# Optimization experiments

Hardware: AMD Instinct MI355X
Metric: run time of the kernel (lower is better)

The kernel has to match this reference:

```python
import jax, jax.numpy as jnp
import numpy as np

D = 128          # latent_dim
N = 40000        # num nodes
B = 8            # num graphs in batch
S = N // B       # nodes per graph
K = 6            # knn
E = 640000       # spatial edges
FF = 256         # ffn hidden


def glorot(key, shape):
    lim = jnp.sqrt(6.0 / (shape[0] + shape[-1]))
    return jax.random.uniform(key, shape, minval=-lim, maxval=lim, dtype=jnp.float32)


def setup_inputs() -> dict:
    key = jax.random.key(0)
    ks = jax.random.split(key, 24)
    inp = {
        "x": jax.random.normal(ks[0], (N, D), dtype=jnp.float32),
        "edge_index": jax.random.randint(ks[1], (2, E), 0, N, dtype=jnp.int64),
        "edge_attr": jax.random.uniform(ks[2], (E, 1), dtype=jnp.float32),
        "batch": jnp.repeat(jnp.arange(B, dtype=jnp.int64), S),
        # spatial GATv2Conv params
        "W_sl": glorot(ks[3], (D, D)), "b_sl": jnp.zeros((D,), jnp.float32),
        "W_sr": glorot(ks[4], (D, D)), "b_sr": jnp.zeros((D,), jnp.float32),
        "att_s": glorot(ks[5], (D,)), "W_se": glorot(ks[6], (1, D)),
        "bias_s": jnp.zeros((D,), jnp.float32),
        # latent GATv2Conv params (no edge features)
        "W_ll": glorot(ks[7], (D, D)), "b_ll": jnp.zeros((D,), jnp.float32),
        "W_lr": glorot(ks[8], (D, D)), "b_lr": jnp.zeros((D,), jnp.float32),
        "att_l": glorot(ks[9], (D,)), "bias_l": jnp.zeros((D,), jnp.float32),
        # concat_skip fusion linear: in = 2*D
        "W_c": glorot(ks[10], (2 * D, D)), "b_c": jnp.zeros((D,), jnp.float32),
        # FFN
        "W_f1": glorot(ks[11], (D, FF)), "b_f1": jnp.zeros((FF,), jnp.float32),
        "W_f2": glorot(ks[12], (FF, D)), "b_f2": jnp.zeros((D,), jnp.float32),
    }
    return inp


def relu6(v):
    return jnp.clip(v, 0.0, 6.0)


def segment_softmax(logits, seg, num_segments):
    m = jax.ops.segment_max(logits, seg, num_segments=num_segments)
    e = jnp.exp(logits - m[seg])
    s = jax.ops.segment_sum(e, seg, num_segments=num_segments)
    return e / s[seg]


def gatv2(x, src, dst, edge_feat, W_l, b_l, W_r, b_r, att, bias):
    """PyG GATv2Conv, heads=1, concat=True, negative_slope=0.2."""
    xl = x @ W_l + b_l            # [N,D] source transform
    xr = x @ W_r + b_r            # [N,D] target transform
    h = xl[src] + xr[dst]         # [E,D]
    if edge_feat is not None:
        h = h + edge_feat         # [E,D] already projected by lin_edge
    h = jax.nn.leaky_relu(h, 0.2)
    alpha = h @ att               # [E]
    alpha = segment_softmax(alpha, dst, N)
    out = jax.ops.segment_sum(xl[src] * alpha[:, None], dst, num_segments=N)
    return out + bias


def knn_edges(x):
    """knn_graph(k=K, loop=False, flow='source_to_target') per graph, plus
    the self loops that latent GATv2Conv adds (add_self_loops=True)."""
    xs = jax.lax.stop_gradient(x).reshape(B, S, D)
    sq = jnp.sum(xs * xs, axis=-1)                       # [B,S]
    d2 = sq[:, :, None] + sq[:, None, :] - 2.0 * jnp.einsum('bid,bjd->bij', xs, xs)
    d2 = jnp.where(jnp.eye(S, dtype=bool)[None], jnp.inf, d2)
    _, idx = jax.lax.top_k(-d2, K)                       # [B,S,K] neighbor ids
    offs = (jnp.arange(B) * S)[:, None, None]
    src = (idx + offs).reshape(-1)                       # neighbors -> sources
    dst = jnp.repeat(jnp.arange(N), K)                   # query nodes -> targets
    loop = jnp.arange(N)
    return jnp.concatenate([src, loop]), jnp.concatenate([dst, loop])


def reference(x, edge_index, edge_attr, batch,
              W_sl, b_sl, W_sr, b_sr, att_s, W_se, bias_s,
              W_ll, b_ll, W_lr, b_lr, att_l, bias_l,
              W_c, b_c, W_f1, b_f1, W_f2, b_f2):
    # spatial channel: GATv2 with scalar edge attr
    e_feat = edge_attr @ W_se                            # lin_edge, [E,D]
    ch_sp = gatv2(x, edge_index[0], edge_index[1], e_feat,
                  W_sl, b_sl, W_sr, b_sr, att_s, bias_s)
    # latent channel: dynamic kNN graph + GATv2
    src_l, dst_l = knn_edges(x)
    ch_lat = gatv2(x, src_l, dst_l, None,
                   W_ll, b_ll, W_lr, b_lr, att_l, bias_l)
    # fusion = concat_skip
    fused = jnp.concatenate([ch_sp, ch_lat], axis=-1) @ W_c + b_c + x
    # FFN block (norms are Identity), residual
    ffn = relu6(fused @ W_f1 + b_f1) @ W_f2 + b_f2
    out = fused + ffn
    # plain_last=False -> final activation relu6
    return relu6(out)
```

## Files before the change

### kernel.cpp

```cpp
#include <hip/hip_runtime.h>
#include <math.h>

constexpr int N  = 40000;
constexpr int D  = 128;
constexpr int E  = 640000;
constexpr int Bg = 8;
constexpr int Sg = 5000;
constexpr int KN = 6;
constexpr int FF = 256;
constexpr int QLEN = 1280;
constexpr int NCAND = 48;

typedef short short8 __attribute__((ext_vector_type(8)));
typedef float f32x4  __attribute__((ext_vector_type(4)));
typedef __attribute__((address_space(1))) const void* gvp;
typedef __attribute__((address_space(3))) void* lvp;

__device__ __forceinline__ unsigned short f2bf(float f)
{
    unsigned int u = __float_as_uint(f);
    return (unsigned short)((u + 0x7fffu + ((u >> 16) & 1u)) >> 16);
}

__device__ __forceinline__ unsigned umin2(unsigned a, unsigned b) { return a < b ? a : b; }

__global__ __launch_bounds__(256) void w_prep_k(
    const float* __restrict__ W0, const float* __restrict__ W1,
    const float* __restrict__ W2, const float* __restrict__ W3,
    const float* __restrict__ Wc, const float* __restrict__ Wf1,
    const float* __restrict__ Wf2,
    unsigned short* __restrict__ wt4, unsigned short* __restrict__ wtc,
    unsigned short* __restrict__ wtf1, unsigned short* __restrict__ wtf2)
{
    int idx = blockIdx.x * 256 + threadIdx.x;
    if (idx < 65536) {
        int m = idx >> 14, rem = idx & 16383;
        int k = rem & 127, c = rem >> 7;
        const float* Wm = (m == 0) ? W0 : (m == 1) ? W1 : (m == 2) ? W2 : W3;
        wt4[m * 16384 + c * 128 + k] = f2bf(Wm[k * 128 + c]);
    } else if (idx < 98304) {
        int rem = idx - 65536; int k = rem & 255, c = rem >> 8;
        wtc[c * 256 + k] = f2bf(Wc[k * 128 + c]);
    } else if (idx < 131072) {
        int rem = idx - 98304; int k = rem & 127, c = rem >> 7;
        wtf1[c * 128 + k] = f2bf(Wf1[k * 256 + c]);
    } else {
        int rem = idx - 131072; int k = rem & 255, c = rem >> 8;
        wtf2[c * 256 + k] = f2bf(Wf2[k * 128 + c]);
    }
}

__global__ __launch_bounds__(256) void gemm_mfma_k(
    const float* __restrict__ A, int lda,
    const unsigned short* __restrict__ Wt, int Kdim,
    const float* __restrict__ bias,
    const float* __restrict__ res,
    float* __restrict__ out, int ldo, int act)
{
    __shared__ float xs[64][36];
    __shared__ unsigned short ws[128][40];
    int tid = threadIdx.x;
    int w = tid >> 6, lane = tid & 63;
    int lg = lane >> 4, ln = lane & 15;
    int r0 = blockIdx.x * 64;
    int cb = blockIdx.y * 128;

    f32x4 acc[8];
#pragma unroll
    for (int ct = 0; ct < 8; ++ct) acc[ct] = {0.f, 0.f, 0.f, 0.f};

    int srow = tid >> 2, sk8 = (tid & 3) * 8;
    int wcol = tid >> 1, wk = (tid & 1) * 16;

    for (int kt = 0; kt < Kdim; kt += 32) {
        __syncthreads();
        *(float4*)&xs[srow][sk8]     = *(const float4*)&A[(size_t)(r0 + srow) * lda + kt + sk8];
        *(float4*)&xs[srow][sk8 + 4] = *(const float4*)&A[(size_t)(r0 + srow) * lda + kt + sk8 + 4];
        *(short8*)&ws[wcol][wk]     = *(const short8*)&Wt[(size_t)(cb + wcol) * Kdim + kt + wk];
        *(short8*)&ws[wcol][wk + 8] = *(const short8*)&Wt[(size_t)(cb + wcol) * Kdim + kt + wk + 8];
        __syncthreads();

        int arow = w * 16 + ln;
        f32x4 a0 = *(const f32x4*)&xs[arow][lg * 8];
        f32x4 a1 = *(const f32x4*)&xs[arow][lg * 8 + 4];
        float af[8] = {a0[0], a0[1], a0[2], a0[3], a1[0], a1[1], a1[2], a1[3]};
        short8 ah, al;
#pragma unroll
        for (int i = 0; i < 8; ++i) {
            unsigned short h = f2bf(af[i]);
            ah[i] = (short)h;
            float hf = __uint_as_float(((unsigned)h) << 16);
            al[i] = (short)f2bf(af[i] - hf);
        }
#pragma unroll
        for (int ct = 0; ct < 8; ++ct) {
            short8 bw = *(const short8*)&ws[ct * 16 + ln][lg * 8];
            acc[ct] = __builtin_amdgcn_mfma_f32_16x16x32_bf16(ah, bw, acc[ct], 0, 0, 0);
            acc[ct] = __builtin_amdgcn_mfma_f32_16x16x32_bf16(al, bw, acc[ct], 0, 0, 0);
        }
    }

#pragma unroll
    for (int ct = 0; ct < 8; ++ct) {
        int c = cb + ct * 16 + ln;
        float bv = bias[c];
#pragma unroll
        for (int rg = 0; rg < 4; ++rg) {
            int r = r0 + w * 16 + lg * 4 + rg;
            float v = acc[ct][rg] + bv;
            if (res) v += res[(size_t)r * 128 + c];
            if (act) v = fminf(fmaxf(v, 0.f), 6.f);
            out[(size_t)r * ldo + c] = v;
        }
    }
}

__global__ __launch_bounds__(256) void gemm4_mfma_k(
    const float* __restrict__ A, const unsigned short* __restrict__ wt4,
    const float* __restrict__ b0, const float* __restrict__ b1,
    const float* __restrict__ b2, const float* __restrict__ b3,
    float* __restrict__ o0, float* __restrict__ o1,
    float* __restrict__ o2, float* __restrict__ o3)
{
    const unsigned short* Wt = wt4 + blockIdx.y * 16384;
    const float* bias; float* out;
    if (blockIdx.y == 0)      { bias = b0; out = o0; }
    else if (blockIdx.y == 1) { bias = b1; out = o1; }
    else if (blockIdx.y == 2) { bias = b2; out = o2; }
    else                      { bias = b3; out = o3; }

    __shared__ float xs[64][36];
    __shared__ unsigned short ws[128][40];
    int tid = threadIdx.x;
    int w = tid >> 6, lane = tid & 63;
    int lg = lane >> 4, ln = lane & 15;
    int r0 = blockIdx.x * 64;

    f32x4 acc[8];
#pragma unroll
    for (int ct = 0; ct < 8; ++ct) acc[ct] = {0.f, 0.f, 0.f, 0.f};

    int srow = tid >> 2, sk8 = (tid & 3) * 8;
    int wcol = tid >> 1, wk = (tid & 1) * 16;

    for (int kt = 0; kt < 128; kt += 32) {
        __syncthreads();
        *(float4*)&xs[srow][sk8]     = *(const float4*)&A[(size_t)(r0 + srow) * 128 + kt + sk8];
        *(float4*)&xs[srow][sk8 + 4] = *(const float4*)&A[(size_t)(r0 + srow) * 128 + kt + sk8 + 4];
        *(short8*)&ws[wcol][wk]     = *(const short8*)&Wt[(size_t)wcol * 128 + kt + wk];
        *(short8*)&ws[wcol][wk + 8] = *(const short8*)&Wt[(size_t)wcol * 128 + kt + wk + 8];
        __syncthreads();

        int arow = w * 16 + ln;
        f32x4 a0 = *(const f32x4*)&xs[arow][lg * 8];
        f32x4 a1 = *(const f32x4*)&xs[arow][lg * 8 + 4];
        float af[8] = {a0[0], a0[1], a0[2], a0[3], a1[0], a1[1], a1[2], a1[3]};
        short8 ah, al;
#pragma unroll
        for (int i = 0; i < 8; ++i) {
            unsigned short h = f2bf(af[i]);
            ah[i] = (short)h;
            float hf = __uint_as_float(((unsigned)h) << 16);
            al[i] = (short)f2bf(af[i] - hf);
        }
#pragma unroll
        for (int ct = 0; ct < 8; ++ct) {
            short8 bw = *(const short8*)&ws[ct * 16 + ln][lg * 8];
            acc[ct] = __builtin_amdgcn_mfma_f32_16x16x32_bf16(ah, bw, acc[ct], 0, 0, 0);
            acc[ct] = __builtin_amdgcn_mfma_f32_16x16x32_bf16(al, bw, acc[ct], 0, 0, 0);
        }
    }

#pragma unroll
    for (int ct = 0; ct < 8; ++ct) {
        int c = ct * 16 + ln;
        float bv = bias[c];
#pragma unroll
        for (int rg = 0; rg < 4; ++rg) {
            int r = r0 + w * 16 + lg * 4 + rg;
            out[(size_t)r * 128 + c] = acc[ct][rg] + bv;
        }
    }
}

__global__ __launch_bounds__(256) void prep_k(const float* __restrict__ x,
                                              unsigned short* __restrict__ xh,
                                              float* __restrict__ sqn)
{
    int w = threadIdx.x >> 6, lane = threadIdx.x & 63;
    int row = blockIdx.x * 4 + w;
    float2 v = *(const float2*)&x[(size_t)row * 128 + lane * 2];
    ushort2 h = make_ushort2(f2bf(v.x), f2bf(v.y));
    *(ushort2*)&xh[(size_t)row * 128 + lane * 2] = h;
    float s = fmaf(v.y, v.y, v.x * v.x);
#pragma unroll
    for (int off = 32; off; off >>= 1) s += __shfl_xor(s, off);
    if (lane == 0) sqn[row] = s;
}

__device__ __forceinline__ void ins6(unsigned (&d)[6], unsigned k)
{
#pragma unroll
    for (int t = 0; t < 6; ++t) {
        unsigned lo = d[t] < k ? d[t] : k;
        unsigned hi = d[t] < k ? k : d[t];
        d[t] = lo; k = hi;
    }
}

__global__ __launch_bounds__(256) void knn_mfma_k(const unsigned short* __restrict__ xh,
                                                  const float* __restrict__ sqn,
                                                  int* __restrict__ cand)
{
    __shared__ char lds[33280];

    int b = blockIdx.x;
    int g = b & 7, r = b >> 3;
    int qtr = r & 3, qblk = r >> 2;
    int gbase = g * Sg;
    int cbase = qtr * QLEN;
    int qlen = (qtr < 3) ? QLEN : (Sg - 3 * QLEN);
    int ntiles = (qlen + 63) >> 6;
    int tid = threadIdx.x;
    int w = tid >> 6, lane = tid & 63;
    int lg = lane >> 4, ln = lane & 15;
    int q0 = qblk * 128 + w * 32;

    short8 bh[2][4];
#pragma unroll
    for (int s = 0; s < 2; ++s) {
        int q = q0 + s * 16 + ln;
        int qrow = gbase + (q < Sg ? q : Sg - 1);
#pragma unroll
        for (int ks = 0; ks < 4; ++ks)
            bh[s][ks] = *(const short8*)&xh[(size_t)qrow * 128 + ks * 32 + lg * 8];
    }

    auto stage = [&](int t64, int buf) {
        int c0 = cbase + t64 * 64;
#pragma unroll
        for (int i = 0; i < 4; ++i) {
            int row = i * 16 + (tid >> 4);
            int cr = c0 + row;
            if (cr >= Sg) cr = Sg - 1;
            int sslot = (tid & 15) ^ (row & 7);
            const unsigned short* src = &xh[(size_t)(gbase + cr) * 128 + sslot * 8];
            char* dst = lds + buf * 16384 + i * 4096 + (tid & 192) * 16;
            __builtin_amdgcn_global_load_lds((gvp)src, (lvp)dst, 16, 0, 0);
        }
        if (tid < 64) {
            int cl = c0 + tid;
            float* cs = (float*)(lds + 32768 + buf * 256);
            cs[tid] = (cl < cbase + qlen) ? (sqn[gbase + cl] + 1024.0f) : __builtin_inff();
        }
    };

    unsigned d6a[6], d6b[6];
#pragma unroll
    for (int t = 0; t < 6; ++t) { d6a[t] = 0xFFFFFFFFu; d6b[t] = 0xFFFFFFFFu; }

    stage(0, 0);
    __syncthreads();

    for (int t64 = 0; t64 < ntiles; ++t64) {
        int cur = t64 & 1;
        if (t64 + 1 < ntiles) stage(t64 + 1, cur ^ 1);
        const char* ldsH = lds + cur * 16384;
        const float* cs_s = (const float*)(lds + 32768 + cur * 256);
        int c0 = cbase + t64 * 64;

#pragma unroll
        for (int g16 = 0; g16 < 4; ++g16) {
            f32x4 acc0 = {0.f, 0.f, 0.f, 0.f};
            f32x4 acc1 = {0.f, 0.f, 0.f, 0.f};
            int rr = g16 * 16 + ln;
            int rsw = (ln & 7) << 4;
#pragma unroll
            for (int ks = 0; ks < 4; ++ks) {
                short8 ah = *(const short8*)(ldsH + rr * 256 + ((lg * 16 + ks * 64) ^ rsw));
                acc0 = __builtin_amdgcn_mfma_f32_16x16x32_bf16(ah, bh[0][ks], acc0, 0, 0, 0);
                acc1 = __builtin_amdgcn_mfma_f32_16x16x32_bf16(ah, bh[1][ks], acc1, 0, 0, 0);
            }
            f32x4 cv = *(const f32x4*)&cs_s[g16 * 16 + lg * 4];
            int idx0 = (c0 - cbase) + g16 * 16 + lg * 4;
            unsigned kb0[4], kb1[4];
#pragma unroll
            for (int rg = 0; rg < 4; ++rg) {
                kb0[rg] = __float_as_uint(fmaf(-2.f, acc0[rg], cv[rg]));
                kb1[rg] = __float_as_uint(fmaf(-2.f, acc1[rg], cv[rg]));
            }
            unsigned mn0 = umin2(umin2(kb0[0], kb0[1]), umin2(kb0[2], kb0[3]));
            unsigned mn1 = umin2(umin2(kb1[0], kb1[1]), umin2(kb1[2], kb1[3]));
            if ((mn0 & 0xFFFFF800u) < d6a[5]) {
#pragma unroll
                for (int rg = 0; rg < 4; ++rg) {
                    unsigned k = (kb0[rg] & 0xFFFFF800u) | (unsigned)(idx0 + rg);
                    if (k < d6a[5]) ins6(d6a, k);
                }
            }
            if ((mn1 & 0xFFFFF800u) < d6b[5]) {
#pragma unroll
                for (int rg = 0; rg < 4; ++rg) {
                    unsigned k = (kb1[rg] & 0xFFFFF800u) | (unsigned)(idx0 + rg);
                    if (k < d6b[5]) ins6(d6b, k);
                }
            }
        }
        __syncthreads();
    }

#pragma unroll
    for (int s = 0; s < 2; ++s) {
        unsigned m12[12];
#pragma unroll
        for (int t = 0; t < 6; ++t) m12[t] = s ? d6b[t] : d6a[t];
#pragma unroll
        for (int t = 6; t < 12; ++t) m12[t] = 0xFFFFFFFFu;
#pragma unroll
        for (int sg = 1; sg < 4; ++sg)
#pragma unroll
            for (int t = 0; t < 6; ++t) {
                unsigned v = __shfl(s ? d6b[t] : d6a[t], ln + sg * 16);
#pragma unroll
                for (int u = 0; u < 12; ++u) {
                    unsigned lo = m12[u] < v ? m12[u] : v;
                    unsigned hi = m12[u] < v ? v : m12[u];
                    m12[u] = lo; v = hi;
                }
            }
        int q = q0 + s * 16 + ln;
        if (lg == 0 && q < Sg) {
            int* cp = &cand[(size_t)(gbase + q) * NCAND + qtr * 12];
#pragma unroll
            for (int t = 0; t < 12; ++t) cp[t] = gbase + cbase + (int)(m12[t] & 2047u);
        }
    }
}

__global__ __launch_bounds__(256) void knn_rerank_k(const float* __restrict__ x,
                                                    const float* __restrict__ sqn,
                                                    const int* __restrict__ cand,
                                                    int* __restrict__ knn_idx)
{
    int w = threadIdx.x >> 6, lane = threadIdx.x & 63;
    int grp = lane >> 4, gl = lane & 15;
    int q = blockIdx.x * 4 + w;
    float4 qa = *(const float4*)&x[(size_t)q * 128 + gl * 8];
    float4 qb = *(const float4*)&x[(size_t)q * 128 + gl * 8 + 4];
    const int* cp = &cand[(size_t)q * NCAND + grp * 12];

    float d6[6]; int i6[6]; float mx = __builtin_inff(); int sl = 0;
#pragma unroll
    for (int t = 0; t < 6; ++t) { d6[t] = __builtin_inff(); i6[t] = -1; }

#pragma unroll 2
    for (int j = 0; j < 12; ++j) {
        int c = cp[j];
        bool ok = (unsigned)c < (unsigned)N && c != q;
        int ca = ok ? c : 0;
        float4 va = *(const float4*)&x[(size_t)ca * 128 + gl * 8];
        float4 vb = *(const float4*)&x[(size_t)ca * 128 + gl * 8 + 4];
        float p = qa.x * va.x;
        p = fmaf(qa.y, va.y, p); p = fmaf(qa.z, va.z, p); p = fmaf(qa.w, va.w, p);
        p = fmaf(qb.x, vb.x, p); p = fmaf(qb.y, vb.y, p);
        p = fmaf(qb.z, vb.z, p); p = fmaf(qb.w, vb.w, p);
#pragma unroll
        for (int off = 1; off < 16; off <<= 1) p += __shfl_xor(p, off);
        float dv = ok ? fmaf(-2.f, p, sqn[ca]) : __builtin_inff();
        if (dv < mx) {
#pragma unroll
            for (int t = 0; t < 6; ++t)
                if (t == sl) { d6[t] = dv; i6[t] = c; }
            float m2 = d6[0]; int s2 = 0;
#pragma unroll
            for (int t = 1; t < 6; ++t)
                if (d6[t] > m2) { m2 = d6[t]; s2 = t; }
            mx = m2; sl = s2;
        }
    }

#pragma unroll
    for (int sg = 1; sg < 4; ++sg) {
#pragma unroll
        for (int t = 0; t < 6; ++t) {
            float dv = __shfl(d6[t], gl + sg * 16);
            int ci = __shfl(i6[t], gl + sg * 16);
            if (grp == 0 && dv < mx) {
#pragma unroll
                for (int u = 0; u < 6; ++u)
                    if (u == sl) { d6[u] = dv; i6[u] = ci; }
                float m2 = d6[0]; int s2 = 0;
#pragma unroll
                for (int u = 1; u < 6; ++u)
                    if (d6[u] > m2) { m2 = d6[u]; s2 = u; }
                mx = m2; sl = s2;
            }
        }
    }
    if (lane < 6) {
        int v;
#pragma unroll
        for (int t = 0; t < 6; ++t) if (t == lane) v = i6[t];
        knn_idx[(size_t)q * 6 + lane] = v;
    }
}

__global__ __launch_bounds__(256) void hist_k(const int* __restrict__ dstA, int* __restrict__ deg)
{
    int e = blockIdx.x * 256 + threadIdx.x;
    atomicAdd(&deg[dstA[e]], 1);
}

__global__ __launch_bounds__(1024) void scan_k(const int* __restrict__ deg, int* __restrict__ rowptr)
{
    __shared__ int ps[1024];
    int t = threadIdx.x;
    const int chunk = 40;
    int base = t * chunk;
    int s = 0;
    for (int k = 0; k < chunk; ++k) { int i = base + k; if (i < N) s += deg[i]; }
    ps[t] = s;
    __syncthreads();
    for (int off = 1; off < 1024; off <<= 1) {
        int v = (t >= off) ? ps[t - off] : 0;
        __syncthreads();
        ps[t] += v;
        __syncthreads();
    }
    int run = ps[t] - s;
    for (int k = 0; k < chunk; ++k) {
        int i = base + k;
        if (i < N) { rowptr[i] = run; run += deg[i]; }
    }
    if (t == 0) rowptr[N] = E;
}

__global__ __launch_bounds__(256) void scatter_k(const int* __restrict__ srcA, const int* __restrict__ dstA,
                                                 const float* __restrict__ ea,
                                                 const int* __restrict__ rowptr, int* __restrict__ cnt,
                                                 int* __restrict__ csr_src, float* __restrict__ csr_ea)
{
    int e = blockIdx.x * 256 + threadIdx.x;
    int d = dstA[e];
    int pos = rowptr[d] + atomicAdd(&cnt[d], 1);
    csr_src[pos] = srcA[e];
    csr_ea[pos] = ea[e];
}

__global__ __launch_bounds__(256) void spatial_gat_k(
    const float* __restrict__ xl, const float* __restrict__ xr,
    const int* __restrict__ rowptr, const int* __restrict__ csr_src, const float* __restrict__ csr_ea,
    const float* __restrict__ att, const float* __restrict__ wse, const float* __restrict__ bias,
    float* __restrict__ ch2)
{
    int w = threadIdx.x >> 6, lane = threadIdx.x & 63;
    int dst = blockIdx.x * 4 + w;
    int base = rowptr[dst];
    int deg = rowptr[dst + 1] - base;
    float xr0 = xr[(size_t)dst * 128 + lane], xr1 = xr[(size_t)dst * 128 + 64 + lane];
    float at0 = att[lane], at1 = att[64 + lane];
    float we0 = wse[lane], we1 = wse[64 + lane];

    float m = -1e30f, ssum = 0.f, o0 = 0.f, o1 = 0.f;
    for (int i = 0; i < deg; ++i) {
        int s = csr_src[base + i];
        float ea = csr_ea[base + i];
        float v0 = xl[(size_t)s * 128 + lane];
        float v1 = xl[(size_t)s * 128 + 64 + lane];
        float h0 = fmaf(ea, we0, v0 + xr0);
        float h1 = fmaf(ea, we1, v1 + xr1);
        h0 = h0 > 0.f ? h0 : 0.2f * h0;
        h1 = h1 > 0.f ? h1 : 0.2f * h1;
        float p = fmaf(h1, at1, h0 * at0);
#pragma unroll
        for (int off = 32; off; off >>= 1) p += __shfl_xor(p, off);
        if (p <= m) {
            float wt = __expf(p - m);
            ssum += wt;
            o0 = fmaf(wt, v0, o0);
            o1 = fmaf(wt, v1, o1);
        } else {
            float sc = __expf(m - p);
            ssum = fmaf(ssum, sc, 1.f);
            o0 = fmaf(o0, sc, v0);
            o1 = fmaf(o1, sc, v1);
            m = p;
        }
    }
    float inv = deg > 0 ? 1.f / ssum : 0.f;
    ch2[(size_t)dst * 256 + lane]      = fmaf(o0, inv, bias[lane]);
    ch2[(size_t)dst * 256 + 64 + lane] = fmaf(o1, inv, bias[64 + lane]);
}

__global__ __launch_bounds__(256) void latent_gat_k(
    const float* __restrict__ xl, const float* __restrict__ xr,
    const int* __restrict__ knn, const float* __restrict__ att,
    const float* __restrict__ bias, float* __restrict__ ch2)
{
    int w = threadIdx.x >> 6, lane = threadIdx.x & 63;
    int dst = blockIdx.x * 4 + w;
    float xr0 = xr[(size_t)dst * 128 + lane], xr1 = xr[(size_t)dst * 128 + 64 + lane];
    float at0 = att[lane], at1 = att[64 + lane];
    int s[7];
#pragma unroll
    for (int j = 0; j < 6; ++j) s[j] = knn[(size_t)dst * 6 + j];
    s[6] = dst;
    float l[7];
#pragma unroll
    for (int j = 0; j < 7; ++j) {
        float h0 = xl[(size_t)s[j] * 128 + lane] + xr0;
        float h1 = xl[(size_t)s[j] * 128 + 64 + lane] + xr1;
        h0 = h0 > 0.f ? h0 : 0.2f * h0;
        h1 = h1 > 0.f ? h1 : 0.2f * h1;
        float p = h0 * at0 + h1 * at1;
#pragma unroll
        for (int off = 32; off; off >>= 1) p += __shfl_xor(p, off);
        l[j] = p;
    }
    float m = l[0];
#pragma unroll
    for (int j = 1; j < 7; ++j) m = fmaxf(m, l[j]);
    float sum = 0.f;
#pragma unroll
    for (int j = 0; j < 7; ++j) { l[j] = __expf(l[j] - m); sum += l[j]; }
    float inv = 1.f / sum;
    float o0 = 0.f, o1 = 0.f;
#pragma unroll
    for (int j = 0; j < 7; ++j) {
        float a = l[j] * inv;
        o0 = fmaf(a, xl[(size_t)s[j] * 128 + lane], o0);
        o1 = fmaf(a, xl[(size_t)s[j] * 128 + 64 + lane], o1);
    }
    ch2[(size_t)dst * 256 + 128 + lane] = o0 + bias[lane];
    ch2[(size_t)dst * 256 + 192 + lane] = o1 + bias[64 + lane];
}

extern "C" void kernel_launch(void* const* d_in, const int* in_sizes, int n_in,
                              void* d_out, int out_size, void* d_ws, size_t ws_size,
                              hipStream_t stream)
{
    const float* x      = (const float*)d_in[0];
    const int*   ei     = (const int*)  d_in[1];
    const float* eattr  = (const float*)d_in[2];
    const float* W_sl   = (const float*)d_in[4];
    const float* b_sl   = (const float*)d_in[5];
    const float* W_sr   = (const float*)d_in[6];
    const float* b_sr   = (const float*)d_in[7];
    const float* att_s  = (const float*)d_in[8];
    const float* W_se   = (const float*)d_in[9];
    const float* bias_s = (const float*)d_in[10];
    const float* W_ll   = (const float*)d_in[11];
    const float* b_ll   = (const float*)d_in[12];
    const float* W_lr   = (const float*)d_in[13];
    const float* b_lr   = (const float*)d_in[14];
    const float* att_l  = (const float*)d_in[15];
    const float* bias_l = (const float*)d_in[16];
    const float* W_c    = (const float*)d_in[17];
    const float* b_c    = (const float*)d_in[18];
    const float* W_f1   = (const float*)d_in[19];
    const float* b_f1   = (const float*)d_in[20];
    const float* W_f2   = (const float*)d_in[21];
    const float* b_f2   = (const float*)d_in[22];
    float* out = (float*)d_out;

    char* wp = (char*)d_ws;
    auto take = [&](size_t bytes) { char* p = wp; wp += (bytes + 255) & ~(size_t)255; return p; };
    float* xl_s    = (float*)take((size_t)N * D * 4);
    float* xr_s    = (float*)take((size_t)N * D * 4);
    float* xl_l    = (float*)take((size_t)N * D * 4);
    float* xr_l    = (float*)take((size_t)N * D * 4);
    float* ch2     = (float*)take((size_t)N * 2 * D * 4);
    float* sqn     = (float*)take((size_t)N * 4);
    int*   knn_idx = (int*)  take((size_t)N * KN * 4);
    int*   deg     = (int*)  take((size_t)N * 4);
    int*   rowptr  = (int*)  take((size_t)(N + 1) * 4);
    int*   csr_src = (int*)  take((size_t)E * 4);
    float* csr_ea  = (float*)take((size_t)E * 4);
    unsigned short* x_hi = (unsigned short*)take((size_t)N * D * 2);
    int*   knn_cand = (int*)take((size_t)N * NCAND * 4);
    unsigned short* wt4  = (unsigned short*)take(65536 * 2);
    unsigned short* wtc  = (unsigned short*)take(32768 * 2);
    unsigned short* wtf1 = (unsigned short*)take(32768 * 2);
    unsigned short* wtf2 = (unsigned short*)take(32768 * 2);
    float* fused   = xl_s;
    float* hbuf    = ch2;
    if ((size_t)(wp - (char*)d_ws) > ws_size) return;

    dim3 blk(256);

    w_prep_k<<<dim3(640), blk, 0, stream>>>(W_sl, W_sr, W_ll, W_lr, W_c, W_f1, W_f2,
                                            wt4, wtc, wtf1, wtf2);

    gemm4_mfma_k<<<dim3(N / 64, 4), blk, 0, stream>>>(x, wt4,
        b_sl, b_sr, b_ll, b_lr, xl_s, xr_s, xl_l, xr_l);

    prep_k<<<dim3(N / 4), blk, 0, stream>>>(x, x_hi, sqn);
    knn_mfma_k<<<dim3(Bg * 40 * 4), blk, 0, stream>>>(x_hi, sqn, knn_cand);
    knn_rerank_k<<<dim3(N / 4), blk, 0, stream>>>(x, sqn, knn_cand, knn_idx);

    hipMemsetAsync(deg, 0, (size_t)N * 4, stream);
    hist_k<<<dim3(E / 256), blk, 0, stream>>>(ei + E, deg);
    scan_k<<<dim3(1), dim3(1024), 0, stream>>>(deg, rowptr);
    hipMemsetAsync(deg, 0, (size_t)N * 4, stream);
    scatter_k<<<dim3(E / 256), blk, 0, stream>>>(ei, ei + E, eattr, rowptr, deg, csr_src, csr_ea);

    spatial_gat_k<<<dim3(N / 4), blk, 0, stream>>>(xl_s, xr_s, rowptr, csr_src, csr_ea,
                                                   att_s, W_se, bias_s, ch2);
    latent_gat_k<<<dim3(N / 4), blk, 0, stream>>>(xl_l, xr_l, knn_idx, att_l, bias_l, ch2);

    gemm_mfma_k<<<dim3(N / 64, 1), blk, 0, stream>>>(ch2, 2 * D, wtc, 256, b_c, x, fused, 128, 0);
    gemm_mfma_k<<<dim3(N / 64, 2), blk, 0, stream>>>(fused, 128, wtf1, 128, b_f1, nullptr, hbuf, 256, 1);
    gemm_mfma_k<<<dim3(N / 64, 1), blk, 0, stream>>>(hbuf, 256, wtf2, 256, b_f2, fused, out, 128, 1);
}
```

Measured before the change: 584.2 us.

## Single-buffer kNN tile staging via registers and merge the two GAT kernels

```diff
diff --git a/kernel.cpp b/kernel.cpp
--- a/kernel.cpp
+++ b/kernel.cpp
@@ -13,8 +13,6 @@
 
 typedef short short8 __attribute__((ext_vector_type(8)));
 typedef float f32x4  __attribute__((ext_vector_type(4)));
-typedef __attribute__((address_space(1))) const void* gvp;
-typedef __attribute__((address_space(3))) void* lvp;
 
 __device__ __forceinline__ unsigned short f2bf(float f)
 {
@@ -212,7 +210,9 @@
                                                   const float* __restrict__ sqn,
                                                   int* __restrict__ cand)
 {
-    __shared__ char lds[33280];
+    __shared__ char lds[16640];
+    char* ldsH = lds;
+    float* cs_s = (float*)(lds + 16384);
 
     int b = blockIdx.x;
     int g = b & 7, r = b >> 3;
@@ -221,6 +221,7 @@
     int cbase = qtr * QLEN;
     int qlen = (qtr < 3) ? QLEN : (Sg - 3 * QLEN);
     int ntiles = (qlen + 63) >> 6;
+    int nfull = (qtr < 3) ? ntiles : ntiles - 1;
     int tid = threadIdx.x;
     int w = tid >> 6, lane = tid & 63;
     int lg = lane >> 4, ln = lane & 15;
@@ -236,39 +237,50 @@
             bh[s][ks] = *(const short8*)&xh[(size_t)qrow * 128 + ks * 32 + lg * 8];
     }
 
-    auto stage = [&](int t64, int buf) {
+    int srow = tid >> 4, sslot = tid & 15;
+    int sw_st = (srow & 7) << 4;
+    int dstoff[4];
+    const unsigned short* src[4];
+#pragma unroll
+    for (int i = 0; i < 4; ++i) {
+        int row = i * 16 + srow;
+        dstoff[i] = row * 256 + ((sslot * 16) ^ sw_st);
+        src[i] = &xh[(size_t)(gbase + cbase + row) * 128 + sslot * 8];
+    }
+    const float* csrc = &sqn[gbase + cbase];
+
+    unsigned d6a[6], d6b[6];
+#pragma unroll
+    for (int t = 0; t < 6; ++t) { d6a[t] = 0xFFFFFFFFu; d6b[t] = 0xFFFFFFFFu; }
+
+    for (int t64 = 0; t64 < ntiles; ++t64) {
+        __syncthreads();
+        if (t64 < nfull) {
+#pragma unroll
+            for (int i = 0; i < 4; ++i) {
+                short8 vh = *(const short8*)src[i];
+                src[i] += 64 * 128;
+                *(short8*)(ldsH + dstoff[i]) = vh;
+            }
+            if (tid < 64) cs_s[tid] = csrc[tid] + 1024.0f;
+        } else {
+            int c0 = cbase + t64 * 64;
+#pragma unroll
+            for (int i = 0; i < 4; ++i) {
+                int cr = c0 + i * 16 + srow;
+                if (cr >= Sg) cr = Sg - 1;
+                short8 vh = *(const short8*)&xh[(size_t)(gbase + cr) * 128 + sslot * 8];
+                *(short8*)(ldsH + dstoff[i]) = vh;
+            }
+            if (tid < 64) {
+                int cl = c0 + tid;
+                cs_s[tid] = (cl < cbase + qlen) ? (sqn[gbase + cl] + 1024.0f) : __builtin_inff();
+            }
+        }
+        csrc += 64;
+        __syncthreads();
+
         int c0 = cbase + t64 * 64;
-#pragma unroll
-        for (int i = 0; i < 4; ++i) {
-            int row = i * 16 + (tid >> 4);
-            int cr = c0 + row;
-            if (cr >= Sg) cr = Sg - 1;
-            int sslot = (tid & 15) ^ (row & 7);
-            const unsigned short* src = &xh[(size_t)(gbase + cr) * 128 + sslot * 8];
-            char* dst = lds + buf * 16384 + i * 4096 + (tid & 192) * 16;
-            __builtin_amdgcn_global_load_lds((gvp)src, (lvp)dst, 16, 0, 0);
-        }
-        if (tid < 64) {
-            int cl = c0 + tid;
-            float* cs = (float*)(lds + 32768 + buf * 256);
-            cs[tid] = (cl < cbase + qlen) ? (sqn[gbase + cl] + 1024.0f) : __builtin_inff();
-        }
-    };
-
-    unsigned d6a[6], d6b[6];
-#pragma unroll
-    for (int t = 0; t < 6; ++t) { d6a[t] = 0xFFFFFFFFu; d6b[t] = 0xFFFFFFFFu; }
-
-    stage(0, 0);
-    __syncthreads();
-
-    for (int t64 = 0; t64 < ntiles; ++t64) {
-        int cur = t64 & 1;
-        if (t64 + 1 < ntiles) stage(t64 + 1, cur ^ 1);
-        const char* ldsH = lds + cur * 16384;
-        const float* cs_s = (const float*)(lds + 32768 + cur * 256);
-        int c0 = cbase + t64 * 64;
-
 #pragma unroll
         for (int g16 = 0; g16 < 4; ++g16) {
             f32x4 acc0 = {0.f, 0.f, 0.f, 0.f};
@@ -306,7 +318,6 @@
                 }
             }
         }
-        __syncthreads();
     }
 
 #pragma unroll
@@ -447,92 +458,89 @@
     csr_ea[pos] = ea[e];
 }
 
-__global__ __launch_bounds__(256) void spatial_gat_k(
-    const float* __restrict__ xl, const float* __restrict__ xr,
+__global__ __launch_bounds__(256) void gat_fused_k(
+    const float* __restrict__ xl_s, const float* __restrict__ xr_s,
     const int* __restrict__ rowptr, const int* __restrict__ csr_src, const float* __restrict__ csr_ea,
-    const float* __restrict__ att, const float* __restrict__ wse, const float* __restrict__ bias,
+    const float* __restrict__ att_s, const float* __restrict__ wse, const float* __restrict__ bias_s,
+    const float* __restrict__ xl_l, const float* __restrict__ xr_l,
+    const int* __restrict__ knn, const float* __restrict__ att_l, const float* __restrict__ bias_l,
     float* __restrict__ ch2)
 {
     int w = threadIdx.x >> 6, lane = threadIdx.x & 63;
     int dst = blockIdx.x * 4 + w;
-    int base = rowptr[dst];
-    int deg = rowptr[dst + 1] - base;
-    float xr0 = xr[(size_t)dst * 128 + lane], xr1 = xr[(size_t)dst * 128 + 64 + lane];
-    float at0 = att[lane], at1 = att[64 + lane];
-    float we0 = wse[lane], we1 = wse[64 + lane];
-
-    float m = -1e30f, ssum = 0.f, o0 = 0.f, o1 = 0.f;
-    for (int i = 0; i < deg; ++i) {
-        int s = csr_src[base + i];
-        float ea = csr_ea[base + i];
-        float v0 = xl[(size_t)s * 128 + lane];
-        float v1 = xl[(size_t)s * 128 + 64 + lane];
-        float h0 = fmaf(ea, we0, v0 + xr0);
-        float h1 = fmaf(ea, we1, v1 + xr1);
-        h0 = h0 > 0.f ? h0 : 0.2f * h0;
-        h1 = h1 > 0.f ? h1 : 0.2f * h1;
-        float p = fmaf(h1, at1, h0 * at0);
-#pragma unroll
-        for (int off = 32; off; off >>= 1) p += __shfl_xor(p, off);
-        if (p <= m) {
-            float wt = __expf(p - m);
-            ssum += wt;
-            o0 = fmaf(wt, v0, o0);
-            o1 = fmaf(wt, v1, o1);
-        } else {
-            float sc = __expf(m - p);
-            ssum = fmaf(ssum, sc, 1.f);
-            o0 = fmaf(o0, sc, v0);
-            o1 = fmaf(o1, sc, v1);
-            m = p;
-        }
-    }
-    float inv = deg > 0 ? 1.f / ssum : 0.f;
-    ch2[(size_t)dst * 256 + lane]      = fmaf(o0, inv, bias[lane]);
-    ch2[(size_t)dst * 256 + 64 + lane] = fmaf(o1, inv, bias[64 + lane]);
-}
-
-__global__ __launch_bounds__(256) void latent_gat_k(
-    const float* __restrict__ xl, const float* __restrict__ xr,
-    const int* __restrict__ knn, const float* __restrict__ att,
-    const float* __restrict__ bias, float* __restrict__ ch2)
-{
-    int w = threadIdx.x >> 6, lane = threadIdx.x & 63;
-    int dst = blockIdx.x * 4 + w;
-    float xr0 = xr[(size_t)dst * 128 + lane], xr1 = xr[(size_t)dst * 128 + 64 + lane];
-    float at0 = att[lane], at1 = att[64 + lane];
-    int s[7];
-#pragma unroll
-    for (int j = 0; j < 6; ++j) s[j] = knn[(size_t)dst * 6 + j];
-    s[6] = dst;
-    float l[7];
-#pragma unroll
-    for (int j = 0; j < 7; ++j) {
-        float h0 = xl[(size_t)s[j] * 128 + lane] + xr0;
-        float h1 = xl[(size_t)s[j] * 128 + 64 + lane] + xr1;
-        h0 = h0 > 0.f ? h0 : 0.2f * h0;
-        h1 = h1 > 0.f ? h1 : 0.2f * h1;
-        float p = h0 * at0 + h1 * at1;
-#pragma unroll
-        for (int off = 32; off; off >>= 1) p += __shfl_xor(p, off);
-        l[j] = p;
-    }
-    float m = l[0];
-#pragma unroll
-    for (int j = 1; j < 7; ++j) m = fmaxf(m, l[j]);
-    float sum = 0.f;
-#pragma unroll
-    for (int j = 0; j < 7; ++j) { l[j] = __expf(l[j] - m); sum += l[j]; }
-    float inv = 1.f / sum;
-    float o0 = 0.f, o1 = 0.f;
-#pragma unroll
-    for (int j = 0; j < 7; ++j) {
-        float a = l[j] * inv;
-        o0 = fmaf(a, xl[(size_t)s[j] * 128 + lane], o0);
-        o1 = fmaf(a, xl[(size_t)s[j] * 128 + 64 + lane], o1);
-    }
-    ch2[(size_t)dst * 256 + 128 + lane] = o0 + bias[lane];
-    ch2[(size_t)dst * 256 + 192 + lane] = o1 + bias[64 + lane];
+
+    if (blockIdx.y == 0) {
+        int base = rowptr[dst];
+        int deg = rowptr[dst + 1] - base;
+        float xr0 = xr_s[(size_t)dst * 128 + lane], xr1 = xr_s[(size_t)dst * 128 + 64 + lane];
+        float at0 = att_s[lane], at1 = att_s[64 + lane];
+        float we0 = wse[lane], we1 = wse[64 + lane];
+
+        float m = -1e30f, ssum = 0.f, o0 = 0.f, o1 = 0.f;
+        for (int i = 0; i < deg; ++i) {
+            int s = csr_src[base + i];
+            float ea = csr_ea[base + i];
+            float v0 = xl_s[(size_t)s * 128 + lane];
+            float v1 = xl_s[(size_t)s * 128 + 64 + lane];
+            float h0 = fmaf(ea, we0, v0 + xr0);
+            float h1 = fmaf(ea, we1, v1 + xr1);
+            h0 = h0 > 0.f ? h0 : 0.2f * h0;
+            h1 = h1 > 0.f ? h1 : 0.2f * h1;
+            float p = fmaf(h1, at1, h0 * at0);
+#pragma unroll
+            for (int off = 32; off; off >>= 1) p += __shfl_xor(p, off);
+            if (p <= m) {
+                float wt = __expf(p - m);
+                ssum += wt;
+                o0 = fmaf(wt, v0, o0);
+                o1 = fmaf(wt, v1, o1);
+            } else {
+                float sc = __expf(m - p);
+                ssum = fmaf(ssum, sc, 1.f);
+                o0 = fmaf(o0, sc, v0);
+                o1 = fmaf(o1, sc, v1);
+                m = p;
+            }
+        }
+        float inv = deg > 0 ? 1.f / ssum : 0.f;
+        ch2[(size_t)dst * 256 + lane]      = fmaf(o0, inv, bias_s[lane]);
+        ch2[(size_t)dst * 256 + 64 + lane] = fmaf(o1, inv, bias_s[64 + lane]);
+    } else {
+        float xr0 = xr_l[(size_t)dst * 128 + lane], xr1 = xr_l[(size_t)dst * 128 + 64 + lane];
+        float at0 = att_l[lane], at1 = att_l[64 + lane];
+        int s[7];
+#pragma unroll
+        for (int j = 0; j < 6; ++j) s[j] = knn[(size_t)dst * 6 + j];
+        s[6] = dst;
+        float l[7];
+#pragma unroll
+        for (int j = 0; j < 7; ++j) {
+            float h0 = xl_l[(size_t)s[j] * 128 + lane] + xr0;
+            float h1 = xl_l[(size_t)s[j] * 128 + 64 + lane] + xr1;
+            h0 = h0 > 0.f ? h0 : 0.2f * h0;
+            h1 = h1 > 0.f ? h1 : 0.2f * h1;
+            float p = h0 * at0 + h1 * at1;
+#pragma unroll
+            for (int off = 32; off; off >>= 1) p += __shfl_xor(p, off);
+            l[j] = p;
+        }
+        float m = l[0];
+#pragma unroll
+        for (int j = 1; j < 7; ++j) m = fmaxf(m, l[j]);
+        float sum = 0.f;
+#pragma unroll
+        for (int j = 0; j < 7; ++j) { l[j] = __expf(l[j] - m); sum += l[j]; }
+        float inv = 1.f / sum;
+        float o0 = 0.f, o1 = 0.f;
+#pragma unroll
+        for (int j = 0; j < 7; ++j) {
+            float a = l[j] * inv;
+            o0 = fmaf(a, xl_l[(size_t)s[j] * 128 + lane], o0);
+            o1 = fmaf(a, xl_l[(size_t)s[j] * 128 + 64 + lane], o1);
+        }
+        ch2[(size_t)dst * 256 + 128 + lane] = o0 + bias_l[lane];
+        ch2[(size_t)dst * 256 + 192 + lane] = o1 + bias_l[64 + lane];
+    }
 }
 
 extern "C" void kernel_launch(void* const* d_in, const int* in_sizes, int n_in,
@@ -604,9 +612,9 @@
     hipMemsetAsync(deg, 0, (size_t)N * 4, stream);
     scatter_k<<<dim3(E / 256), blk, 0, stream>>>(ei, ei + E, eattr, rowptr, deg, csr_src, csr_ea);
 
-    spatial_gat_k<<<dim3(N / 4), blk, 0, stream>>>(xl_s, xr_s, rowptr, csr_src, csr_ea,
-                                                   att_s, W_se, bias_s, ch2);
-    latent_gat_k<<<dim3(N / 4), blk, 0, stream>>>(xl_l, xr_l, knn_idx, att_l, bias_l, ch2);
+    gat_fused_k<<<dim3(N / 4, 2), blk, 0, stream>>>(xl_s, xr_s, rowptr, csr_src, csr_ea,
+                                                    att_s, W_se, bias_s,
+                                                    xl_l, xr_l, knn_idx, att_l, bias_l, ch2);
 
     gemm_mfma_k<<<dim3(N / 64, 1), blk, 0, stream>>>(ch2, 2 * D, wtc, 256, b_c, x, fused, 128, 0);
     gemm_mfma_k<<<dim3(N / 64, 2), blk, 0, stream>>>(fused, 128, wtf1, 128, b_f1, nullptr, hbuf, 256, 1);
```

Result: faster. 570.6 us (-2.3%).
